# Optimization experiments

Measured on AMD Instinct MI355X. Metric: run time of the kernel, lower is better.

The kernel has to match this reference:

```python
import jax, jax.numpy as jnp
import numpy as np

S = 80.0          # feature_size
LAMBDA_COORD = 5.0
LAMBDA_NOOBJ = 0.5


def setup_inputs() -> dict:
    key = jax.random.key(0)
    k1, k2, k3 = jax.random.split(key, 3)
    pred_tensor = jax.random.uniform(k1, (1024, 80, 80, 5), dtype=jnp.float32)
    target_boxes = jax.random.uniform(k2, (1024, 80, 80, 4), dtype=jnp.float32)
    obj_mask = jax.random.randint(k3, (1024, 80, 80), 0, 2, dtype=jnp.int32)
    return {"pred_tensor": pred_tensor, "target_boxes": target_boxes, "obj_mask": obj_mask}


def _xyxy(w, h):
    # Faithful to the original (buggy) conversion: pred_xyxy[:, :2] = pred[:, 2]/S - 0.5*pred[:, 2:4]
    # i.e. the 'center' used for BOTH x and y is w/S.
    c = w / S
    return c - 0.5 * w, c - 0.5 * h, c + 0.5 * w, c + 0.5 * h


def reference(pred_tensor, target_boxes, obj_mask):
    # pred_tensor: [N, 80, 80, 5]  (x, y, w, h, conf), target_boxes: [N, 80, 80, 4]
    m = (obj_mask > 0).astype(pred_tensor.dtype)        # coord_mask; (1-m) is noobj_mask
    px, py, pw, ph, pc = (pred_tensor[..., i] for i in range(5))
    tx, ty, tw, th = (target_boxes[..., i] for i in range(4))

    # per-cell 1x1 IoU (B=1, so the response-assignment loop is trivial: mask always 1)
    px1, py1, px2, py2 = _xyxy(pw, ph)
    tx1, ty1, tx2, ty2 = _xyxy(tw, th)
    iw = jnp.maximum(jnp.minimum(px2, tx2) - jnp.maximum(px1, tx1), 0.0)
    ih = jnp.maximum(jnp.minimum(py2, ty2) - jnp.maximum(py1, ty1), 0.0)
    inter = iw * ih
    union = pw * ph + tw * th - inter
    iou = jax.lax.stop_gradient(inter / union)          # original uses max_iou.data (detached)

    loss_xy = jnp.sum(m * ((px - tx) ** 2 + (py - ty) ** 2))
    loss_wh = jnp.sum(m * ((jnp.sqrt(pw) - jnp.sqrt(tw)) ** 2 + (jnp.sqrt(ph) - jnp.sqrt(th)) ** 2))
    loss_obj = jnp.sum(m * (pc - iou) ** 2)
    loss_noobj = jnp.sum((1.0 - m) * pc ** 2)           # noobj target conf is 0

    batch = pred_tensor.shape[0]
    loss = (LAMBDA_COORD * (loss_xy + loss_wh) + loss_obj + LAMBDA_NOOBJ * loss_noobj) / batch
    return loss
```

## Files before the change

### kernel.cpp

```cpp
#include <hip/hip_runtime.h>


#define S_INV (1.0f / 80.0f)

__global__ void zero_out_kernel(float* out) {
    out[0] = 0.0f;
}

__global__ __launch_bounds__(256) void yolo_loss_kernel(
    const float4* __restrict__ pred4,
    const float4* __restrict__ targ4,
    const int4*  __restrict__ mask4,
    float* __restrict__ out,
    int ngroups)
{
    float acc = 0.0f;
    int tid = blockIdx.x * blockDim.x + threadIdx.x;
    int stride = gridDim.x * blockDim.x;

    for (int g = tid; g < ngroups; g += stride) {
        float p[20];
        float t[16];
        float4 v;
        v = pred4[5 * g + 0]; p[ 0] = v.x; p[ 1] = v.y; p[ 2] = v.z; p[ 3] = v.w;
        v = pred4[5 * g + 1]; p[ 4] = v.x; p[ 5] = v.y; p[ 6] = v.z; p[ 7] = v.w;
        v = pred4[5 * g + 2]; p[ 8] = v.x; p[ 9] = v.y; p[10] = v.z; p[11] = v.w;
        v = pred4[5 * g + 3]; p[12] = v.x; p[13] = v.y; p[14] = v.z; p[15] = v.w;
        v = pred4[5 * g + 4]; p[16] = v.x; p[17] = v.y; p[18] = v.z; p[19] = v.w;
        v = targ4[4 * g + 0]; t[ 0] = v.x; t[ 1] = v.y; t[ 2] = v.z; t[ 3] = v.w;
        v = targ4[4 * g + 1]; t[ 4] = v.x; t[ 5] = v.y; t[ 6] = v.z; t[ 7] = v.w;
        v = targ4[4 * g + 2]; t[ 8] = v.x; t[ 9] = v.y; t[10] = v.z; t[11] = v.w;
        v = targ4[4 * g + 3]; t[12] = v.x; t[13] = v.y; t[14] = v.z; t[15] = v.w;
        int4 mi = mask4[g];
        int mm[4] = { mi.x, mi.y, mi.z, mi.w };

        #pragma unroll
        for (int j = 0; j < 4; ++j) {
            float px = p[5 * j + 0], py = p[5 * j + 1], pw = p[5 * j + 2];
            float ph = p[5 * j + 3], pc = p[5 * j + 4];
            float tx = t[4 * j + 0], ty = t[4 * j + 1], tw = t[4 * j + 2], th = t[4 * j + 3];

            float cp = pw * S_INV;
            float ct = tw * S_INV;
            float px1 = cp - 0.5f * pw, py1 = cp - 0.5f * ph;
            float px2 = cp + 0.5f * pw, py2 = cp + 0.5f * ph;
            float tx1 = ct - 0.5f * tw, ty1 = ct - 0.5f * th;
            float tx2 = ct + 0.5f * tw, ty2 = ct + 0.5f * th;

            float iw = fmaxf(fminf(px2, tx2) - fmaxf(px1, tx1), 0.0f);
            float ih = fmaxf(fminf(py2, ty2) - fmaxf(py1, ty1), 0.0f);
            float inter = iw * ih;
            float uni = pw * ph + tw * th - inter;
            float iou = inter / uni;

            float dx = px - tx, dy = py - ty;
            float sw = sqrtf(pw) - sqrtf(tw);
            float sh = sqrtf(ph) - sqrtf(th);
            float dobj = pc - iou;

            float obj_term = 5.0f * ((dx * dx + dy * dy) + (sw * sw + sh * sh)) + dobj * dobj;
            float noobj_term = 0.5f * pc * pc;
            acc += (mm[j] > 0) ? obj_term : noobj_term;
        }
    }

    #pragma unroll
    for (int off = 32; off > 0; off >>= 1)
        acc += __shfl_down(acc, off, 64);

    __shared__ float wsum[4];
    int lane = threadIdx.x & 63;
    int wid = threadIdx.x >> 6;
    if (lane == 0) wsum[wid] = acc;
    __syncthreads();

    if (threadIdx.x == 0) {
        float b = wsum[0] + wsum[1] + wsum[2] + wsum[3];
        atomicAdd(out, b * (1.0f / 1024.0f));
    }
}

extern "C" void kernel_launch(void* const* d_in, const int* in_sizes, int n_in,
                              void* d_out, int out_size, void* d_ws, size_t ws_size,
                              hipStream_t stream) {
    const float4* pred4 = (const float4*)d_in[0];
    const float4* targ4 = (const float4*)d_in[1];
    const int4*   mask4 = (const int4*)d_in[2];
    float* out = (float*)d_out;

    int ncells = in_sizes[2];
    int ngroups = ncells / 4;

    zero_out_kernel<<<1, 1, 0, stream>>>(out);

    const int block = 256;
    const int grid = 2048;
    yolo_loss_kernel<<<grid, block, 0, stream>>>(pred4, targ4, mask4, out, ngroups);
}
```

Before: 57.09 us.

## Stage prediction tiles into LDS with async double-buffered global_load_lds pipeline

Prediction data is now copied per tile straight into shared memory with async global_load_lds, so each wave issues fully coalesced 16-byte loads instead of the 80-byte strided per-thread reads. Two LDS buffers hold consecutive tiles, so the next tile's loads and the target/mask loads overlap with compute on the current one, using explicit vmcnt waits and barriers. The final reduction drops the shared-memory stage and does one atomic per wave. This adds barrier overhead, needs tile counts that divide evenly, and relies on the hand-tuned vmcnt(10) count being right.

New measurement: 127.2 us. 2.23x slower.

```diff
diff --git a/kernel.cpp b/kernel.cpp
--- a/kernel.cpp
+++ b/kernel.cpp
@@ -1,99 +1,179 @@
 #include <hip/hip_runtime.h>
+#include <stdint.h>
 
 
 #define S_INV (1.0f / 80.0f)
 
-__global__ void zero_out_kernel(float* out) {
-    out[0] = 0.0f;
+typedef float f4 __attribute__((ext_vector_type(4)));
+typedef int   i4 __attribute__((ext_vector_type(4)));
+
+#define TILE_GROUPS 256
+#define PRED_TILE_B (TILE_GROUPS * 80)
+
+__global__ void zero_out_kernel(float* out) { out[0] = 0.0f; }
+
+__device__ __forceinline__ void async16(const void* g, void* l) {
+    __builtin_amdgcn_global_load_lds(
+        (const __attribute__((address_space(1))) void*)g,
+        (__attribute__((address_space(3))) void*)l, 16, 0, 0);
+}
+
+#define PIPE_WAIT_BARRIER_10() do {                          \
+    asm volatile("s_waitcnt vmcnt(10)" ::: "memory");        \
+    __builtin_amdgcn_s_barrier();                            \
+    asm volatile("" ::: "memory");                           \
+} while (0)
+
+#define PIPE_WAIT_BARRIER_0() do {                           \
+    asm volatile("s_waitcnt vmcnt(0)" ::: "memory");         \
+    __builtin_amdgcn_s_barrier();                            \
+    asm volatile("" ::: "memory");                           \
+} while (0)
+
+#define PIPE_END_BARRIER() do {                              \
+    asm volatile("s_waitcnt lgkmcnt(0)" ::: "memory");       \
+    __builtin_amdgcn_s_barrier();                            \
+    asm volatile("" ::: "memory");                           \
+} while (0)
+
+struct TM { f4 t0, t1, t2, t3; i4 m; };
+
+__device__ __forceinline__ void load_tm(TM& tm, const f4* __restrict__ targ4,
+                                        const i4* __restrict__ mask4, int gid) {
+    tm.t0 = targ4[4 * gid + 0];
+    tm.t1 = targ4[4 * gid + 1];
+    tm.t2 = targ4[4 * gid + 2];
+    tm.t3 = targ4[4 * gid + 3];
+    tm.m  = mask4[gid];
+}
+
+__device__ __forceinline__ void stage_pred(const char* __restrict__ predB, char* buf,
+                                           int tile, int wave, int lane) {
+    const char* src = predB + (size_t)tile * PRED_TILE_B;
+    #pragma unroll
+    for (int i = 0; i < 5; ++i) {
+        int off = (i * 4 + wave) * 1024;
+        async16(src + off + lane * 16, buf + off);
+    }
+}
+
+__device__ __forceinline__ float cell_loss(float px, float py, float pw, float ph, float pc,
+                                           float tx, float ty, float tw, float th, int m)
+{
+    float cp = pw * S_INV;
+    float ct = tw * S_INV;
+    float px1 = cp - 0.5f * pw, py1 = cp - 0.5f * ph;
+    float px2 = cp + 0.5f * pw, py2 = cp + 0.5f * ph;
+    float tx1 = ct - 0.5f * tw, ty1 = ct - 0.5f * th;
+    float tx2 = ct + 0.5f * tw, ty2 = ct + 0.5f * th;
+
+    float iw = fmaxf(fminf(px2, tx2) - fmaxf(px1, tx1), 0.0f);
+    float ih = fmaxf(fminf(py2, ty2) - fmaxf(py1, ty1), 0.0f);
+    float inter = iw * ih;
+    float uni = pw * ph + tw * th - inter;
+    float iou = inter / uni;
+
+    float dx = px - tx, dy = py - ty;
+    float sw = sqrtf(pw) - sqrtf(tw);
+    float sh = sqrtf(ph) - sqrtf(th);
+    float dobj = pc - iou;
+
+    float obj_term = 5.0f * ((dx * dx + dy * dy) + (sw * sw + sh * sh)) + dobj * dobj;
+    float noobj_term = 0.5f * pc * pc;
+    return (m > 0) ? obj_term : noobj_term;
+}
+
+__device__ __forceinline__ float compute_tile(const char* smem_base, const TM& tm, int t) {
+    const f4* lp = (const f4*)(smem_base + t * 80);
+    f4 p0 = lp[0], p1 = lp[1], p2 = lp[2], p3 = lp[3], p4 = lp[4];
+    float s = 0.0f;
+    s += cell_loss(p0.x, p0.y, p0.z, p0.w, p1.x,
+                   tm.t0.x, tm.t0.y, tm.t0.z, tm.t0.w, tm.m.x);
+    s += cell_loss(p1.y, p1.z, p1.w, p2.x, p2.y,
+                   tm.t1.x, tm.t1.y, tm.t1.z, tm.t1.w, tm.m.y);
+    s += cell_loss(p2.z, p2.w, p3.x, p3.y, p3.z,
+                   tm.t2.x, tm.t2.y, tm.t2.z, tm.t2.w, tm.m.z);
+    s += cell_loss(p3.w, p4.x, p4.y, p4.z, p4.w,
+                   tm.t3.x, tm.t3.y, tm.t3.z, tm.t3.w, tm.m.w);
+    return s;
 }
 
 __global__ __launch_bounds__(256) void yolo_loss_kernel(
-    const float4* __restrict__ pred4,
-    const float4* __restrict__ targ4,
-    const int4*  __restrict__ mask4,
+    const char* __restrict__ predB,
+    const f4*  __restrict__ targ4,
+    const i4*  __restrict__ mask4,
     float* __restrict__ out,
-    int ngroups)
+    int ntiles)
 {
+    __shared__ char smem[2 * PRED_TILE_B];
+
+    const int t    = threadIdx.x;
+    const int lane = t & 63;
+    const int wave = t >> 6;
+    const int stride = gridDim.x;
     float acc = 0.0f;
-    int tid = blockIdx.x * blockDim.x + threadIdx.x;
-    int stride = gridDim.x * blockDim.x;
 
-    for (int g = tid; g < ngroups; g += stride) {
-        float p[20];
-        float t[16];
-        float4 v;
-        v = pred4[5 * g + 0]; p[ 0] = v.x; p[ 1] = v.y; p[ 2] = v.z; p[ 3] = v.w;
-        v = pred4[5 * g + 1]; p[ 4] = v.x; p[ 5] = v.y; p[ 6] = v.z; p[ 7] = v.w;
-        v = pred4[5 * g + 2]; p[ 8] = v.x; p[ 9] = v.y; p[10] = v.z; p[11] = v.w;
-        v = pred4[5 * g + 3]; p[12] = v.x; p[13] = v.y; p[14] = v.z; p[15] = v.w;
-        v = pred4[5 * g + 4]; p[16] = v.x; p[17] = v.y; p[18] = v.z; p[19] = v.w;
-        v = targ4[4 * g + 0]; t[ 0] = v.x; t[ 1] = v.y; t[ 2] = v.z; t[ 3] = v.w;
-        v = targ4[4 * g + 1]; t[ 4] = v.x; t[ 5] = v.y; t[ 6] = v.z; t[ 7] = v.w;
-        v = targ4[4 * g + 2]; t[ 8] = v.x; t[ 9] = v.y; t[10] = v.z; t[11] = v.w;
-        v = targ4[4 * g + 3]; t[12] = v.x; t[13] = v.y; t[14] = v.z; t[15] = v.w;
-        int4 mi = mask4[g];
-        int mm[4] = { mi.x, mi.y, mi.z, mi.w };
+    int idx = blockIdx.x;
+    const int cnt = (ntiles - 1 - idx) / stride + 1;
 
-        #pragma unroll
-        for (int j = 0; j < 4; ++j) {
-            float px = p[5 * j + 0], py = p[5 * j + 1], pw = p[5 * j + 2];
-            float ph = p[5 * j + 3], pc = p[5 * j + 4];
-            float tx = t[4 * j + 0], ty = t[4 * j + 1], tw = t[4 * j + 2], th = t[4 * j + 3];
+    TM A, B;
+    stage_pred(predB, smem, idx, wave, lane);
+    load_tm(A, targ4, mask4, idx * TILE_GROUPS + t);
 
-            float cp = pw * S_INV;
-            float ct = tw * S_INV;
-            float px1 = cp - 0.5f * pw, py1 = cp - 0.5f * ph;
-            float px2 = cp + 0.5f * pw, py2 = cp + 0.5f * ph;
-            float tx1 = ct - 0.5f * tw, ty1 = ct - 0.5f * th;
-            float tx2 = ct + 0.5f * tw, ty2 = ct + 0.5f * th;
+    int done = 0;
+    while (done + 2 <= cnt - 1) {
+        int n1 = idx + stride, n2 = idx + 2 * stride;
+        stage_pred(predB, smem + PRED_TILE_B, n1, wave, lane);
+        load_tm(B, targ4, mask4, n1 * TILE_GROUPS + t);
+        PIPE_WAIT_BARRIER_10();
+        acc += compute_tile(smem, A, t);
+        PIPE_END_BARRIER();
 
-            float iw = fmaxf(fminf(px2, tx2) - fmaxf(px1, tx1), 0.0f);
-            float ih = fmaxf(fminf(py2, ty2) - fmaxf(py1, ty1), 0.0f);
-            float inter = iw * ih;
-            float uni = pw * ph + tw * th - inter;
-            float iou = inter / uni;
+        stage_pred(predB, smem, n2, wave, lane);
+        load_tm(A, targ4, mask4, n2 * TILE_GROUPS + t);
+        PIPE_WAIT_BARRIER_10();
+        acc += compute_tile(smem + PRED_TILE_B, B, t);
+        PIPE_END_BARRIER();
 
-            float dx = px - tx, dy = py - ty;
-            float sw = sqrtf(pw) - sqrtf(tw);
-            float sh = sqrtf(ph) - sqrtf(th);
-            float dobj = pc - iou;
+        idx = n2;
+        done += 2;
+    }
+    if (done < cnt - 1) {
+        int n1 = idx + stride;
+        stage_pred(predB, smem + PRED_TILE_B, n1, wave, lane);
+        load_tm(B, targ4, mask4, n1 * TILE_GROUPS + t);
+        PIPE_WAIT_BARRIER_10();
+        acc += compute_tile(smem, A, t);
+        PIPE_END_BARRIER();
 
-            float obj_term = 5.0f * ((dx * dx + dy * dy) + (sw * sw + sh * sh)) + dobj * dobj;
-            float noobj_term = 0.5f * pc * pc;
-            acc += (mm[j] > 0) ? obj_term : noobj_term;
-        }
+        PIPE_WAIT_BARRIER_0();
+        acc += compute_tile(smem + PRED_TILE_B, B, t);
+    } else {
+        PIPE_WAIT_BARRIER_0();
+        acc += compute_tile(smem, A, t);
     }
 
     #pragma unroll
     for (int off = 32; off > 0; off >>= 1)
         acc += __shfl_down(acc, off, 64);
-
-    __shared__ float wsum[4];
-    int lane = threadIdx.x & 63;
-    int wid = threadIdx.x >> 6;
-    if (lane == 0) wsum[wid] = acc;
-    __syncthreads();
-
-    if (threadIdx.x == 0) {
-        float b = wsum[0] + wsum[1] + wsum[2] + wsum[3];
-        atomicAdd(out, b * (1.0f / 1024.0f));
-    }
+    if (lane == 0)
+        atomicAdd(out, acc * (1.0f / 1024.0f));
 }
 
 extern "C" void kernel_launch(void* const* d_in, const int* in_sizes, int n_in,
                               void* d_out, int out_size, void* d_ws, size_t ws_size,
                               hipStream_t stream) {
-    const float4* pred4 = (const float4*)d_in[0];
-    const float4* targ4 = (const float4*)d_in[1];
-    const int4*   mask4 = (const int4*)d_in[2];
+    const char* predB = (const char*)d_in[0];
+    const f4*   targ4 = (const f4*)d_in[1];
+    const i4*   mask4 = (const i4*)d_in[2];
     float* out = (float*)d_out;
 
     int ncells = in_sizes[2];
-    int ngroups = ncells / 4;
+    int ntiles = ncells / (4 * TILE_GROUPS);
 
     zero_out_kernel<<<1, 1, 0, stream>>>(out);
 
     const int block = 256;
     const int grid = 2048;
-    yolo_loss_kernel<<<grid, block, 0, stream>>>(pred4, targ4, mask4, out, ngroups);
+    yolo_loss_kernel<<<grid, block, 0, stream>>>(predB, targ4, mask4, out, ntiles);
 }
```
